# Kernel optimization log

Hardware: AMD Instinct MI355X
Metric: run time of the kernel (lower is better)

Reference implementation:

```python
import jax, jax.numpy as jnp
import numpy as np

B, N, D = 4, 2048, 1024
H = 16
HD = D // H


def setup_inputs() -> dict:
    key = jax.random.key(0)
    ks = jax.random.split(key, 6)
    x = jax.random.normal(ks[0], (B, N, D), dtype=jnp.float32)
    # additive causal mask: 0 on/below diagonal, -inf above
    neg = jnp.float32(-1e9)
    causal_mask = jnp.where(jnp.triu(jnp.ones((N, N), dtype=bool), k=1), neg, 0.0).astype(jnp.float32)
    s = 1.0 / np.sqrt(D)
    Wqkv = jax.random.normal(ks[1], (D, 3 * D), dtype=jnp.float32) * s
    bqkv = jax.random.normal(ks[2], (3 * D,), dtype=jnp.float32) * 0.01
    Wproj = jax.random.normal(ks[3], (D, D), dtype=jnp.float32) * s
    bproj = jax.random.normal(ks[4], (D,), dtype=jnp.float32) * 0.01
    return {"x": x, "causal_mask": causal_mask, "Wqkv": Wqkv, "bqkv": bqkv, "Wproj": Wproj, "bproj": bproj}


def reference(x, causal_mask, Wqkv, bqkv, Wproj, bproj):
    b, n, d = x.shape
    qkv = x @ Wqkv + bqkv  # [B,N,3D]
    qkv = qkv.reshape(b, n, 3, H, HD).transpose(2, 0, 3, 1, 4)  # [3,B,H,N,HD]
    q, k, v = qkv[0], qkv[1], qkv[2]
    scale = HD ** -0.5
    attn = jnp.einsum('bhqd,bhkd->bhqk', q, k) * scale  # [B,H,N,N]
    attn = attn + causal_mask  # broadcast [N,N] -> [B,H,N,N]
    attn = jax.nn.softmax(attn, axis=-1)
    out = jnp.einsum('bhqk,bhkd->bhqd', attn, v)  # [B,H,N,HD]
    out = out.transpose(0, 2, 1, 3).reshape(b, n, d)
    return out @ Wproj + bproj
```

## Files before the change

### kernel.cpp

```cpp
#include <hip/hip_runtime.h>
#include <hip/hip_bf16.h>

typedef unsigned short u16;
typedef unsigned int u32;
typedef __attribute__((ext_vector_type(8))) short bf16x8;
typedef __attribute__((ext_vector_type(4))) float f32x4;

#define AS1(p) ((const __attribute__((address_space(1))) void*)(p))
#define AS3(p) ((__attribute__((address_space(3))) void*)(p))

#if __has_builtin(__builtin_amdgcn_exp2f)
#define EXP2F(x) __builtin_amdgcn_exp2f(x)
#else
#define EXP2F(x) exp2f(x)
#endif

static __device__ __forceinline__ float b2f(u16 u) {
  union { unsigned int i; float f; } v; v.i = ((unsigned int)u) << 16; return v.f;
}
static __device__ __forceinline__ u16 f2b(float f) {
  union { float f; unsigned int i; } v; v.f = f;
  unsigned int r = v.i + 0x7FFFu + ((v.i >> 16) & 1u);
  return (u16)(r >> 16);
}
static __device__ __forceinline__ u32 cvt_pk_bf16(float lo, float hi) {
  u32 r;
  asm("v_cvt_pk_bf16_f32 %0, %1, %2" : "=v"(r) : "v"(lo), "v"(hi));
  return r;
}

__global__ __launch_bounds__(256) void cast_f32_bf16(const float* __restrict__ src,
                                                     u16* __restrict__ dst, int n8) {
  int stride = gridDim.x * blockDim.x;
  for (int i = blockIdx.x * blockDim.x + threadIdx.x; i < n8; i += stride) {
    const float4* s = (const float4*)(src + (size_t)i * 8);
    float4 a = s[0], b = s[1];
    bf16x8 o;
    o[0] = (short)f2b(a.x); o[1] = (short)f2b(a.y); o[2] = (short)f2b(a.z); o[3] = (short)f2b(a.w);
    o[4] = (short)f2b(b.x); o[5] = (short)f2b(b.y); o[6] = (short)f2b(b.z); o[7] = (short)f2b(b.w);
    *(bf16x8*)(dst + (size_t)i * 8) = o;
  }
}

__global__ __launch_bounds__(256) void transpose_w(const float* __restrict__ src,
                                                   u16* __restrict__ dst,
                                                   int R, int C) {
  __shared__ float tile[32][33];
  int c0 = blockIdx.x * 32, r0 = blockIdx.y * 32;
  int tx = threadIdx.x, ty = threadIdx.y;
  for (int i = ty; i < 32; i += 8) tile[i][tx] = src[(size_t)(r0 + i) * C + c0 + tx];
  __syncthreads();
  for (int i = ty; i < 32; i += 8) dst[(size_t)(c0 + i) * R + r0 + tx] = f2b(tile[tx][i]);
}

__global__ __launch_bounds__(256) void transpose_v(const u16* __restrict__ qkv,
                                                   u16* __restrict__ VT) {
  const int N = 2048, TD = 3072, D = 1024;
  int bh = blockIdx.y, n0 = blockIdx.x * 64;
  int b = bh >> 4, h = bh & 15;
  int tid = threadIdx.x;
  __shared__ u16 tl[64][72];
  #pragma unroll
  for (int i = 0; i < 16; ++i) {
    int idx = tid + i * 256;
    int nl = idx >> 6, dd = idx & 63;
    tl[dd][nl] = qkv[(size_t)(b * N + n0 + nl) * TD + 2 * D + h * 64 + dd];
  }
  __syncthreads();
  #pragma unroll
  for (int i = 0; i < 16; ++i) {
    int idx = tid + i * 256;
    int dd = idx >> 6, nl = idx & 63;
    VT[((size_t)bh * 64 + dd) * N + n0 + nl] = tl[dd][nl];
  }
}

template <typename OutT>
__global__ __launch_bounds__(256) void gemm_bt_bias(
    const u16* __restrict__ A,
    const u16* __restrict__ BT,
    const float* __restrict__ bias,
    OutT* __restrict__ C,
    int M, int N, int K) {
  __shared__ alignas(16) u16 Als[128 * 32];
  __shared__ alignas(16) u16 Bls[128 * 32];
  const int m0 = blockIdx.x * 128, n0 = blockIdx.y * 128;
  const int t = threadIdx.x;
  const int w = t >> 6, lane = t & 63;
  const int wr = w >> 1, wc = w & 1;
  const int rlo = lane & 15, g = lane >> 4;

  f32x4 acc[4][4] = {};

  const int r0 = t >> 2;
  const int c0 = (t & 3) << 3;
  const u16* aSrc = A + (size_t)(m0 + r0) * K + c0;
  const u16* bSrc = BT + (size_t)(n0 + r0) * K + c0;

  for (int k0 = 0; k0 < K; k0 += 32) {
    __builtin_amdgcn_global_load_lds(AS1(aSrc + k0), AS3(&Als[t * 8]), 16, 0, 0);
    __builtin_amdgcn_global_load_lds(AS1(aSrc + (size_t)64 * K + k0), AS3(&Als[(t + 256) * 8]), 16, 0, 0);
    __builtin_amdgcn_global_load_lds(AS1(bSrc + k0), AS3(&Bls[t * 8]), 16, 0, 0);
    __builtin_amdgcn_global_load_lds(AS1(bSrc + (size_t)64 * K + k0), AS3(&Bls[(t + 256) * 8]), 16, 0, 0);
    __syncthreads();

    bf16x8 a[4], b[4];
    #pragma unroll
    for (int m = 0; m < 4; ++m)
      a[m] = *(const bf16x8*)&Als[(wr * 64 + m * 16 + rlo) * 32 + g * 8];
    #pragma unroll
    for (int n = 0; n < 4; ++n)
      b[n] = *(const bf16x8*)&Bls[(wc * 64 + n * 16 + rlo) * 32 + g * 8];
    #pragma unroll
    for (int m = 0; m < 4; ++m)
      #pragma unroll
      for (int n = 0; n < 4; ++n)
        acc[m][n] = __builtin_amdgcn_mfma_f32_16x16x32_bf16(a[m], b[n], acc[m][n], 0, 0, 0);
    __syncthreads();
  }

  #pragma unroll
  for (int n = 0; n < 4; ++n) {
    const int col = n0 + wc * 64 + n * 16 + rlo;
    const float bv = bias[col];
    #pragma unroll
    for (int m = 0; m < 4; ++m) {
      const int row = m0 + wr * 64 + m * 16 + g * 4;
      #pragma unroll
      for (int i = 0; i < 4; ++i) {
        float r = acc[m][n][i] + bv;
        if constexpr (sizeof(OutT) == 2)
          C[(size_t)(row + i) * N + col] = (OutT)f2b(r);
        else
          C[(size_t)(row + i) * N + col] = (OutT)r;
      }
    }
  }
}

__global__ __launch_bounds__(256) void attn_fwd(
    const u16* __restrict__ qkv,
    const u16* __restrict__ VT,
    u16* __restrict__ O) {
  const int N = 2048, TD = 3072, D = 1024;
  const int bid = blockIdx.x;
  const int qp = bid >> 6, bh = bid & 63;
  const int b = bh >> 4, h = bh & 15;
  const int t = threadIdx.x, w = t >> 6, lane = t & 63;
  const int rlo = lane & 15, g = lane >> 4;
  const int qbase[2] = {qp * 64 + w * 16, (31 - qp) * 64 + w * 16};

  __shared__ alignas(16) u16 Kls[64 * 64];
  __shared__ alignas(16) u16 Vls[64 * 64];
  __shared__ alignas(16) u16 Pls[4][32 * 64];

  bf16x8 qf[2][2];
  #pragma unroll
  for (int m = 0; m < 2; ++m) {
    const u16* qp_ = qkv + ((size_t)(b * N) + qbase[m] + rlo) * TD + h * 64 + g * 8;
    #pragma unroll
    for (int kb = 0; kb < 2; ++kb) {
      bf16x8 v = *(const bf16x8*)(qp_ + kb * 32);
      #pragma unroll
      for (int j = 0; j < 8; ++j)
        v[j] = (short)f2b(b2f((u16)v[j]) * 0.125f);
      qf[m][kb] = v;
    }
  }

  const int c1 = t, c2 = t + 256;
  const int r1 = c1 >> 3, sc1 = ((c1 & 7) ^ (r1 & 7)) * 8;
  const int r2 = c2 >> 3, sc2 = ((c2 & 7) ^ (r2 & 7)) * 8;
  const u16* kbase = qkv + (size_t)(b * N) * TD + D + h * 64;
  const u16* vbase = VT + (size_t)bh * 64 * N;

  f32x4 o_acc[2][4] = {};
  float psum[2] = {0.f, 0.f};
  const int jend = (31 - qp) * 64;

  const float L2E = 1.44269504089f;
  const float NSH = -23.0830992f;

  for (int j0 = 0; j0 <= jend; j0 += 64) {
    __builtin_amdgcn_global_load_lds(AS1(kbase + (size_t)(j0 + r1) * TD + sc1), AS3(&Kls[c1 * 8]), 16, 0, 0);
    __builtin_amdgcn_global_load_lds(AS1(kbase + (size_t)(j0 + r2) * TD + sc2), AS3(&Kls[c2 * 8]), 16, 0, 0);
    __builtin_amdgcn_global_load_lds(AS1(vbase + (size_t)r1 * N + j0 + sc1), AS3(&Vls[c1 * 8]), 16, 0, 0);
    __builtin_amdgcn_global_load_lds(AS1(vbase + (size_t)r2 * N + j0 + sc2), AS3(&Vls[c2 * 8]), 16, 0, 0);
    __syncthreads();

    const bool act0 = (j0 <= qbase[0] + 15);

    f32x4 s[2][4];
    __builtin_amdgcn_s_setprio(1);
    #pragma unroll
    for (int nt = 0; nt < 4; ++nt) {
      const int krow = nt * 16 + rlo;
      const int ksw = (krow & 7) << 3;
      bf16x8 k0 = *(const bf16x8*)&Kls[krow * 64 + ((g * 8) ^ ksw)];
      bf16x8 k1 = *(const bf16x8*)&Kls[krow * 64 + ((32 + g * 8) ^ ksw)];
      f32x4 z1 = {};
      z1 = __builtin_amdgcn_mfma_f32_16x16x32_bf16(k0, qf[1][0], z1, 0, 0, 0);
      z1 = __builtin_amdgcn_mfma_f32_16x16x32_bf16(k1, qf[1][1], z1, 0, 0, 0);
      s[1][nt] = z1;
      if (act0) {
        f32x4 z0 = {};
        z0 = __builtin_amdgcn_mfma_f32_16x16x32_bf16(k0, qf[0][0], z0, 0, 0, 0);
        z0 = __builtin_amdgcn_mfma_f32_16x16x32_bf16(k1, qf[0][1], z0, 0, 0, 0);
        s[0][nt] = z0;
      }
    }
    __builtin_amdgcn_s_setprio(0);

    #pragma unroll
    for (int m = 0; m < 2; ++m) {
      if (m == 0 && !act0) continue;
      if (!(j0 + 63 <= qbase[m])) {
        const int qr = qbase[m] + rlo;
        #pragma unroll
        for (int nt = 0; nt < 4; ++nt) {
          const int kc0 = j0 + nt * 16 + g * 4;
          #pragma unroll
          for (int i = 0; i < 4; ++i)
            if (kc0 + i > qr) s[m][nt][i] = -1e30f;
        }
      }
    }

    #pragma unroll
    for (int m = 0; m < 2; ++m) {
      if (m == 0 && !act0) continue;
      const int prow = m * 16 + rlo;
      const int psw = (prow & 7) << 3;
      #pragma unroll
      for (int nt = 0; nt < 4; ++nt) {
        float p0 = EXP2F(fmaf(s[m][nt][0], L2E, NSH));
        float p1 = EXP2F(fmaf(s[m][nt][1], L2E, NSH));
        float p2 = EXP2F(fmaf(s[m][nt][2], L2E, NSH));
        float p3 = EXP2F(fmaf(s[m][nt][3], L2E, NSH));
        psum[m] += (p0 + p1) + (p2 + p3);
        uint2 pw;
        pw.x = cvt_pk_bf16(p0, p1);
        pw.y = cvt_pk_bf16(p2, p3);
        *(uint2*)&Pls[w][prow * 64 + ((nt * 16 + g * 4) ^ psw)] = pw;
      }
    }

    bf16x8 va[4][2];
    #pragma unroll
    for (int ft = 0; ft < 4; ++ft) {
      const int vrow = ft * 16 + rlo;
      const int vsw = (vrow & 7) << 3;
      va[ft][0] = *(const bf16x8*)&Vls[vrow * 64 + ((g * 8) ^ vsw)];
      va[ft][1] = *(const bf16x8*)&Vls[vrow * 64 + ((32 + g * 8) ^ vsw)];
    }
    {
      const int prow = 16 + rlo;
      const int psw = (prow & 7) << 3;
      bf16x8 pa0 = *(const bf16x8*)&Pls[w][prow * 64 + ((g * 8) ^ psw)];
      bf16x8 pa1 = *(const bf16x8*)&Pls[w][prow * 64 + ((32 + g * 8) ^ psw)];
      __builtin_amdgcn_s_setprio(1);
      #pragma unroll
      for (int ft = 0; ft < 4; ++ft) {
        o_acc[1][ft] = __builtin_amdgcn_mfma_f32_16x16x32_bf16(pa0, va[ft][0], o_acc[1][ft], 0, 0, 0);
        o_acc[1][ft] = __builtin_amdgcn_mfma_f32_16x16x32_bf16(pa1, va[ft][1], o_acc[1][ft], 0, 0, 0);
      }
      __builtin_amdgcn_s_setprio(0);
    }
    if (act0) {
      const int prow = rlo;
      const int psw = (prow & 7) << 3;
      bf16x8 pa0 = *(const bf16x8*)&Pls[w][prow * 64 + ((g * 8) ^ psw)];
      bf16x8 pa1 = *(const bf16x8*)&Pls[w][prow * 64 + ((32 + g * 8) ^ psw)];
      __builtin_amdgcn_s_setprio(1);
      #pragma unroll
      for (int ft = 0; ft < 4; ++ft) {
        o_acc[0][ft] = __builtin_amdgcn_mfma_f32_16x16x32_bf16(pa0, va[ft][0], o_acc[0][ft], 0, 0, 0);
        o_acc[0][ft] = __builtin_amdgcn_mfma_f32_16x16x32_bf16(pa1, va[ft][1], o_acc[0][ft], 0, 0, 0);
      }
      __builtin_amdgcn_s_setprio(0);
    }
    __syncthreads();
  }

  #pragma unroll
  for (int m = 0; m < 2; ++m) {
    float rs = psum[m];
    rs += __shfl_xor(rs, 16, 64);
    rs += __shfl_xor(rs, 32, 64);
    float inv = 1.0f / rs;
    #pragma unroll
    for (int i = 0; i < 4; ++i) {
      float invq = __shfl(inv, g * 4 + i, 64);
      const int qr = qbase[m] + g * 4 + i;
      #pragma unroll
      for (int ft = 0; ft < 4; ++ft)
        O[((size_t)(b * N) + qr) * D + h * 64 + ft * 16 + rlo] = f2b(o_acc[m][ft][i] * invq);
    }
  }
}

extern "C" void kernel_launch(void* const* d_in, const int* in_sizes, int n_in,
                              void* d_out, int out_size, void* d_ws, size_t ws_size,
                              hipStream_t stream) {
  const float* x     = (const float*)d_in[0];
  const float* Wqkv  = (const float*)d_in[2];
  const float* bqkv  = (const float*)d_in[3];
  const float* Wproj = (const float*)d_in[4];
  const float* bproj = (const float*)d_in[5];
  float* out = (float*)d_out;

  const int B = 4, N = 2048, D = 1024, H = 16;
  const int BN = B * N;
  const int TD = 3 * D;

  char* ws = (char*)d_ws;
  u16* qkv    = (u16*)(ws);
  u16* vt     = (u16*)(ws + 50331648);
  u16* aout   = (u16*)(ws + 67108864);
  u16* wqkvT  = (u16*)(ws + 83886080);
  u16* wprojT = (u16*)(ws + 90177536);
  u16* xb     = (u16*)(ws + 92274688);

  cast_f32_bf16<<<2048, 256, 0, stream>>>(x, xb, BN * D / 8);
  transpose_w<<<dim3(TD / 32, D / 32), dim3(32, 8), 0, stream>>>(Wqkv, wqkvT, D, TD);
  transpose_w<<<dim3(D / 32, D / 32), dim3(32, 8), 0, stream>>>(Wproj, wprojT, D, D);
  gemm_bt_bias<u16><<<dim3(BN / 128, TD / 128), 256, 0, stream>>>(xb, wqkvT, bqkv, qkv, BN, TD, D);
  transpose_v<<<dim3(N / 64, B * H), 256, 0, stream>>>(qkv, vt);
  attn_fwd<<<1024, 256, 0, stream>>>(qkv, vt, aout);
  gemm_bt_bias<float><<<dim3(BN / 128, D / 128), 256, 0, stream>>>(aout, wprojT, bproj, out, BN, D, D);
}
```

Baseline: 204.2 us.

## Switch attention to 32x32 MFMA tiles with register-resident P via permlane swap

Reworks the attention kernel to use 32x32x16 bf16 MFMAs, with each wave owning 32 query rows in each of two paired causal tiles. Grid blocks go from 1024 to 512, so each block covers 128 query rows. The softmax probabilities are repacked in registers with v_permlane32_swap instead of a round trip through shared memory, which removes the Pls buffer and its LDS traffic. This cuts LDS reads/writes and MFMA instruction count per tile, but halves the number of blocks and raises register pressure, which may lower occupancy.

New measurement: 219.1 us. +7.3%, slower.

```diff
diff --git a/kernel.cpp b/kernel.cpp
--- a/kernel.cpp
+++ b/kernel.cpp
@@ -5,6 +5,7 @@
 typedef unsigned int u32;
 typedef __attribute__((ext_vector_type(8))) short bf16x8;
 typedef __attribute__((ext_vector_type(4))) float f32x4;
+typedef __attribute__((ext_vector_type(16))) float f32x16;
 
 #define AS1(p) ((const __attribute__((address_space(1))) void*)(p))
 #define AS3(p) ((__attribute__((address_space(3))) void*)(p))
@@ -27,6 +28,9 @@
   u32 r;
   asm("v_cvt_pk_bf16_f32 %0, %1, %2" : "=v"(r) : "v"(lo), "v"(hi));
   return r;
+}
+static __device__ __forceinline__ void permswap(u32& a, u32& b) {
+  asm("v_permlane32_swap_b32 %0, %1" : "+v"(a), "+v"(b));
 }
 
 __global__ __launch_bounds__(256) void cast_f32_bf16(const float* __restrict__ src,
@@ -147,24 +151,23 @@
   const int qp = bid >> 6, bh = bid & 63;
   const int b = bh >> 4, h = bh & 15;
   const int t = threadIdx.x, w = t >> 6, lane = t & 63;
-  const int rlo = lane & 15, g = lane >> 4;
-  const int qbase[2] = {qp * 64 + w * 16, (31 - qp) * 64 + w * 16};
+  const int l31 = lane & 31, hi = lane >> 5;
+  const int qbase[2] = {qp * 128 + w * 32, (15 - qp) * 128 + w * 32};
 
   __shared__ alignas(16) u16 Kls[64 * 64];
   __shared__ alignas(16) u16 Vls[64 * 64];
-  __shared__ alignas(16) u16 Pls[4][32 * 64];
-
-  bf16x8 qf[2][2];
+
+  bf16x8 qf[2][4];
   #pragma unroll
   for (int m = 0; m < 2; ++m) {
-    const u16* qp_ = qkv + ((size_t)(b * N) + qbase[m] + rlo) * TD + h * 64 + g * 8;
-    #pragma unroll
-    for (int kb = 0; kb < 2; ++kb) {
-      bf16x8 v = *(const bf16x8*)(qp_ + kb * 32);
+    const u16* qp_ = qkv + ((size_t)(b * N) + qbase[m] + l31) * TD + h * 64 + hi * 8;
+    #pragma unroll
+    for (int c = 0; c < 4; ++c) {
+      bf16x8 v = *(const bf16x8*)(qp_ + c * 16);
       #pragma unroll
       for (int j = 0; j < 8; ++j)
         v[j] = (short)f2b(b2f((u16)v[j]) * 0.125f);
-      qf[m][kb] = v;
+      qf[m][c] = v;
     }
   }
 
@@ -174,9 +177,9 @@
   const u16* kbase = qkv + (size_t)(b * N) * TD + D + h * 64;
   const u16* vbase = VT + (size_t)bh * 64 * N;
 
-  f32x4 o_acc[2][4] = {};
+  f32x16 o_acc[2][2] = {};
   float psum[2] = {0.f, 0.f};
-  const int jend = (31 - qp) * 64;
+  const int jend = (15 - qp) * 128 + 64;
 
   const float L2E = 1.44269504089f;
   const float NSH = -23.0830992f;
@@ -188,113 +191,88 @@
     __builtin_amdgcn_global_load_lds(AS1(vbase + (size_t)r2 * N + j0 + sc2), AS3(&Vls[c2 * 8]), 16, 0, 0);
     __syncthreads();
 
-    const bool act0 = (j0 <= qbase[0] + 15);
-
-    f32x4 s[2][4];
-    __builtin_amdgcn_s_setprio(1);
-    #pragma unroll
-    for (int nt = 0; nt < 4; ++nt) {
-      const int krow = nt * 16 + rlo;
-      const int ksw = (krow & 7) << 3;
-      bf16x8 k0 = *(const bf16x8*)&Kls[krow * 64 + ((g * 8) ^ ksw)];
-      bf16x8 k1 = *(const bf16x8*)&Kls[krow * 64 + ((32 + g * 8) ^ ksw)];
-      f32x4 z1 = {};
-      z1 = __builtin_amdgcn_mfma_f32_16x16x32_bf16(k0, qf[1][0], z1, 0, 0, 0);
-      z1 = __builtin_amdgcn_mfma_f32_16x16x32_bf16(k1, qf[1][1], z1, 0, 0, 0);
-      s[1][nt] = z1;
-      if (act0) {
-        f32x4 z0 = {};
-        z0 = __builtin_amdgcn_mfma_f32_16x16x32_bf16(k0, qf[0][0], z0, 0, 0, 0);
-        z0 = __builtin_amdgcn_mfma_f32_16x16x32_bf16(k1, qf[0][1], z0, 0, 0, 0);
-        s[0][nt] = z0;
+    const bool act1 = (j0 <= qbase[1] + 31);
+    const bool act0 = (j0 <= qbase[0] + 31);
+
+    if (act1) {
+      bf16x8 kf[2][4];
+      #pragma unroll
+      for (int st = 0; st < 2; ++st) {
+        const int row = st * 32 + l31, sw = (row & 7) << 3;
+        #pragma unroll
+        for (int c = 0; c < 4; ++c)
+          kf[st][c] = *(const bf16x8*)&Kls[row * 64 + ((c * 16 + hi * 8) ^ sw)];
       }
-    }
-    __builtin_amdgcn_s_setprio(0);
-
-    #pragma unroll
-    for (int m = 0; m < 2; ++m) {
-      if (m == 0 && !act0) continue;
-      if (!(j0 + 63 <= qbase[m])) {
-        const int qr = qbase[m] + rlo;
+      bf16x8 vf[2][2][2];
+      #pragma unroll
+      for (int dt = 0; dt < 2; ++dt) {
+        const int row = dt * 32 + l31, sw = (row & 7) << 3;
         #pragma unroll
-        for (int nt = 0; nt < 4; ++nt) {
-          const int kc0 = j0 + nt * 16 + g * 4;
-          #pragma unroll
-          for (int i = 0; i < 4; ++i)
-            if (kc0 + i > qr) s[m][nt][i] = -1e30f;
+        for (int st = 0; st < 2; ++st)
+          #pragma unroll
+          for (int kc = 0; kc < 2; ++kc)
+            vf[st][kc][dt] = *(const bf16x8*)&Vls[row * 64 + ((st * 32 + kc * 16 + hi * 8) ^ sw)];
+      }
+
+      #pragma unroll
+      for (int m = 0; m < 2; ++m) {
+        if (m == 0 && !act0) continue;
+        const int qr = qbase[m] + l31;
+        const bool straddle = !(j0 + 63 <= qbase[m]);
+        #pragma unroll
+        for (int st = 0; st < 2; ++st) {
+          f32x16 S = {};
+          __builtin_amdgcn_s_setprio(1);
+          #pragma unroll
+          for (int c = 0; c < 4; ++c)
+            S = __builtin_amdgcn_mfma_f32_32x32x16_bf16(kf[st][c], qf[m][c], S, 0, 0, 0);
+          __builtin_amdgcn_s_setprio(0);
+          if (straddle) {
+            const int kvb = j0 + st * 32 + 4 * hi;
+            #pragma unroll
+            for (int r = 0; r < 16; ++r)
+              if (kvb + (r & 3) + 8 * (r >> 2) > qr) S[r] = -1e30f;
+          }
+          float p[16];
+          #pragma unroll
+          for (int r = 0; r < 16; ++r) p[r] = EXP2F(fmaf(S[r], L2E, NSH));
+          float ps = 0.f;
+          #pragma unroll
+          for (int r = 0; r < 16; ++r) ps += p[r];
+          psum[m] += ps;
+          u32 wq[8];
+          #pragma unroll
+          for (int i = 0; i < 8; ++i) wq[i] = cvt_pk_bf16(p[2 * i], p[2 * i + 1]);
+          permswap(wq[0], wq[2]); permswap(wq[1], wq[3]);
+          permswap(wq[4], wq[6]); permswap(wq[5], wq[7]);
+          union { u32 u[4]; bf16x8 v; } pa0, pa1;
+          pa0.u[0] = wq[0]; pa0.u[1] = wq[1]; pa0.u[2] = wq[2]; pa0.u[3] = wq[3];
+          pa1.u[0] = wq[4]; pa1.u[1] = wq[5]; pa1.u[2] = wq[6]; pa1.u[3] = wq[7];
+          __builtin_amdgcn_s_setprio(1);
+          #pragma unroll
+          for (int dt = 0; dt < 2; ++dt) {
+            o_acc[m][dt] = __builtin_amdgcn_mfma_f32_32x32x16_bf16(pa0.v, vf[st][0][dt], o_acc[m][dt], 0, 0, 0);
+            o_acc[m][dt] = __builtin_amdgcn_mfma_f32_32x32x16_bf16(pa1.v, vf[st][1][dt], o_acc[m][dt], 0, 0, 0);
+          }
+          __builtin_amdgcn_s_setprio(0);
         }
       }
     }
-
-    #pragma unroll
-    for (int m = 0; m < 2; ++m) {
-      if (m == 0 && !act0) continue;
-      const int prow = m * 16 + rlo;
-      const int psw = (prow & 7) << 3;
-      #pragma unroll
-      for (int nt = 0; nt < 4; ++nt) {
-        float p0 = EXP2F(fmaf(s[m][nt][0], L2E, NSH));
-        float p1 = EXP2F(fmaf(s[m][nt][1], L2E, NSH));
-        float p2 = EXP2F(fmaf(s[m][nt][2], L2E, NSH));
-        float p3 = EXP2F(fmaf(s[m][nt][3], L2E, NSH));
-        psum[m] += (p0 + p1) + (p2 + p3);
-        uint2 pw;
-        pw.x = cvt_pk_bf16(p0, p1);
-        pw.y = cvt_pk_bf16(p2, p3);
-        *(uint2*)&Pls[w][prow * 64 + ((nt * 16 + g * 4) ^ psw)] = pw;
-      }
-    }
-
-    bf16x8 va[4][2];
-    #pragma unroll
-    for (int ft = 0; ft < 4; ++ft) {
-      const int vrow = ft * 16 + rlo;
-      const int vsw = (vrow & 7) << 3;
-      va[ft][0] = *(const bf16x8*)&Vls[vrow * 64 + ((g * 8) ^ vsw)];
-      va[ft][1] = *(const bf16x8*)&Vls[vrow * 64 + ((32 + g * 8) ^ vsw)];
-    }
-    {
-      const int prow = 16 + rlo;
-      const int psw = (prow & 7) << 3;
-      bf16x8 pa0 = *(const bf16x8*)&Pls[w][prow * 64 + ((g * 8) ^ psw)];
-      bf16x8 pa1 = *(const bf16x8*)&Pls[w][prow * 64 + ((32 + g * 8) ^ psw)];
-      __builtin_amdgcn_s_setprio(1);
-      #pragma unroll
-      for (int ft = 0; ft < 4; ++ft) {
-        o_acc[1][ft] = __builtin_amdgcn_mfma_f32_16x16x32_bf16(pa0, va[ft][0], o_acc[1][ft], 0, 0, 0);
-        o_acc[1][ft] = __builtin_amdgcn_mfma_f32_16x16x32_bf16(pa1, va[ft][1], o_acc[1][ft], 0, 0, 0);
-      }
-      __builtin_amdgcn_s_setprio(0);
-    }
-    if (act0) {
-      const int prow = rlo;
-      const int psw = (prow & 7) << 3;
-      bf16x8 pa0 = *(const bf16x8*)&Pls[w][prow * 64 + ((g * 8) ^ psw)];
-      bf16x8 pa1 = *(const bf16x8*)&Pls[w][prow * 64 + ((32 + g * 8) ^ psw)];
-      __builtin_amdgcn_s_setprio(1);
-      #pragma unroll
-      for (int ft = 0; ft < 4; ++ft) {
-        o_acc[0][ft] = __builtin_amdgcn_mfma_f32_16x16x32_bf16(pa0, va[ft][0], o_acc[0][ft], 0, 0, 0);
-        o_acc[0][ft] = __builtin_amdgcn_mfma_f32_16x16x32_bf16(pa1, va[ft][1], o_acc[0][ft], 0, 0, 0);
-      }
-      __builtin_amdgcn_s_setprio(0);
-    }
     __syncthreads();
   }
 
   #pragma unroll
   for (int m = 0; m < 2; ++m) {
-    float rs = psum[m];
-    rs += __shfl_xor(rs, 16, 64);
-    rs += __shfl_xor(rs, 32, 64);
+    float rs = psum[m] + __shfl_xor(psum[m], 32, 64);
     float inv = 1.0f / rs;
     #pragma unroll
-    for (int i = 0; i < 4; ++i) {
-      float invq = __shfl(inv, g * 4 + i, 64);
-      const int qr = qbase[m] + g * 4 + i;
-      #pragma unroll
-      for (int ft = 0; ft < 4; ++ft)
-        O[((size_t)(b * N) + qr) * D + h * 64 + ft * 16 + rlo] = f2b(o_acc[m][ft][i] * invq);
+    for (int r = 0; r < 16; ++r) {
+      const int qrow = (r & 3) + 8 * (r >> 2) + 4 * hi;
+      const float invq = __shfl(inv, qrow, 64);
+      const int q = qbase[m] + qrow;
+      #pragma unroll
+      for (int dt = 0; dt < 2; ++dt)
+        O[((size_t)(b * N) + q) * D + h * 64 + dt * 32 + l31] = f2b(o_acc[m][dt][r] * invq);
     }
   }
 }
@@ -326,6 +304,6 @@
   transpose_w<<<dim3(D / 32, D / 32), dim3(32, 8), 0, stream>>>(Wproj, wprojT, D, D);
   gemm_bt_bias<u16><<<dim3(BN / 128, TD / 128), 256, 0, stream>>>(xb, wqkvT, bqkv, qkv, BN, TD, D);
   transpose_v<<<dim3(N / 64, B * H), 256, 0, stream>>>(qkv, vt);
-  attn_fwd<<<1024, 256, 0, stream>>>(qkv, vt, aout);
+  attn_fwd<<<512, 256, 0, stream>>>(qkv, vt, aout);
   gemm_bt_bias<float><<<dim3(BN / 128, D / 128), 256, 0, stream>>>(aout, wprojT, bproj, out, BN, D, D);
 }
```
